# Kernel optimization log

Measured on AMD Instinct MI355X. Metric: run time of the kernel, lower is better.

The kernel has to match this reference:

```python
import jax, jax.numpy as jnp
import numpy as np

N_NODES = 10000
N_EDGES = 320000
IN_DIM = 128
HID = 256


def setup_inputs() -> dict:
    key = jax.random.key(0)
    ks = jax.random.split(key, 10)
    s_in = 1.0 / np.sqrt(IN_DIM)
    s_h = 1.0 / np.sqrt(HID)
    return {
        "x": jax.random.normal(ks[0], (N_NODES, IN_DIM), dtype=jnp.float32),
        "edge_index": jax.random.randint(ks[1], (2, N_EDGES), 0, N_NODES, dtype=jnp.int64),
        # feature_projector Linear(IN_DIM -> HID)
        "Wp": jax.random.uniform(ks[2], (IN_DIM, HID), jnp.float32, -s_in, s_in),
        "bp": jax.random.uniform(ks[3], (HID,), jnp.float32, -s_in, s_in),
        # LSTM(input=HID, hidden=HID) params, torch layout [4H, H], gate order i,f,g,o
        "W_ih": jax.random.uniform(ks[4], (4 * HID, HID), jnp.float32, -s_h, s_h),
        "W_hh": jax.random.uniform(ks[5], (4 * HID, HID), jnp.float32, -s_h, s_h),
        "b_ih": jax.random.uniform(ks[6], (4 * HID,), jnp.float32, -s_h, s_h),
        "b_hh": jax.random.uniform(ks[7], (4 * HID,), jnp.float32, -s_h, s_h),
        # EvolveGCN-O initial weight [H, H] (glorot-style)
        "initial_weight": jax.random.normal(ks[8], (HID, HID), dtype=jnp.float32) * np.sqrt(2.0 / (2 * HID)),
        # GCNConv bias
        "b_gcn": jnp.zeros((HID,), dtype=jnp.float32),
    }


def _forward(x, edge_index, Wp, bp, W_ih, W_hh, b_ih, b_hh, initial_weight, b_gcn):
    n = x.shape[0]
    # 1) feature projection
    h = x @ Wp + bp  # [N, H]
    # 2) EvolveGCN-O: one LSTM step on the weight matrix (rows = batch),
    #    with h0 = c0 = initial_weight; evolved hidden state is the GCN weight.
    gates = initial_weight @ W_ih.T + b_ih + initial_weight @ W_hh.T + b_hh  # [H, 4H]
    i_g, f_g, g_g, o_g = jnp.split(gates, 4, axis=-1)
    c = jax.nn.sigmoid(f_g) * initial_weight + jax.nn.sigmoid(i_g) * jnp.tanh(g_g)
    W = jax.nn.sigmoid(o_g) * jnp.tanh(c)  # [H, H]
    # 3) GCN propagation with fixed W: out = D^{-1/2}(A+I)D^{-1/2} (h W) + b
    hw = h @ W  # [N, H]
    self_loop = jnp.arange(n, dtype=edge_index.dtype)
    src = jnp.concatenate([edge_index[0], self_loop])
    dst = jnp.concatenate([edge_index[1], self_loop])
    ones = jnp.ones(src.shape[0], dtype=hw.dtype)
    deg = jax.ops.segment_sum(ones, dst, num_segments=n)  # in-degree incl. self loop
    dinv = jnp.where(deg > 0, jax.lax.rsqrt(deg), 0.0)
    norm = dinv[src] * dinv[dst]  # [E+N]
    out = jax.ops.segment_sum(hw[src] * norm[:, None], dst, num_segments=n)
    return out + b_gcn


def reference(x, edge_index, Wp, bp, W_ih, W_hh, b_ih, b_hh, initial_weight, b_gcn):
    return _forward(x, edge_index, Wp, bp, W_ih, W_hh, b_ih, b_hh, initial_weight, b_gcn)
```

## Files before the change

kernel.cpp:

```cpp
#include <hip/hip_runtime.h>
#include <math.h>

#define N_NODES 10000
#define N_EDGES 320000
#define IN_DIM  128
#define HID     256
#define CAP     128

#define NB_GATES 64
#define NB_FILL  1250
#define NB_XCVT  80


__device__ __forceinline__ unsigned bf16rne(float f) {
    union { float f; unsigned u; } c; c.f = f;
    return (c.u + 0x7FFFu + ((c.u >> 16) & 1u)) >> 16;
}

__global__ __launch_bounds__(256)
void k_prep(const int* __restrict__ ei, int* __restrict__ cursor,
            int* __restrict__ bucket, const float* __restrict__ iw,
            const float* __restrict__ wih, const float* __restrict__ whh,
            float* __restrict__ G, const float* __restrict__ x,
            unsigned* __restrict__ xb) {
    __shared__ float smem[8192];
    if (blockIdx.x >= NB_GATES + NB_FILL) {
        int tid = (blockIdx.x - NB_GATES - NB_FILL) * 256 + threadIdx.x;
        const float2* x2 = (const float2*)x;
        #pragma unroll
        for (int it = 0; it < 32; ++it) {
            int idx = tid + it * (NB_XCVT * 256);
            if (idx < N_NODES * 64) {
                float2 v = x2[idx];
                xb[idx] = bf16rne(v.x) | (bf16rne(v.y) << 16);
            }
        }
        return;
    }
    if (blockIdx.x >= NB_GATES) {
        int e = (blockIdx.x - NB_GATES) * 256 + threadIdx.x;
        int s = ei[e];
        int d = ei[N_EDGES + e];
        int pos = atomicAdd(&cursor[d], 1);
        if (pos < CAP) bucket[d * CAP + pos] = s;
        return;
    }
    int bid = blockIdx.x;
    int m0 = (bid & 3) * 64, n0 = (bid >> 2) * 64;
    float (*aT)[64] = (float(*)[64])smem;
    float (*bS)[64] = (float(*)[64])(smem + 4096);
    int t = threadIdx.x;
    int tm = t & 15, tn = t >> 4;
    float acc[4][4] = {};
    for (int kt = 0; kt < 4; ++kt) {
        int k0 = kt * 64;
        int row = t >> 2;
        #pragma unroll
        for (int r = 0; r < 4; ++r) {
            int k4 = 4 * (t & 3) + r;
            float4 av = *(const float4*)&iw[(m0 + row) * HID + k0 + 4 * k4];
            aT[4 * k4 + 0][row] = av.x; aT[4 * k4 + 1][row] = av.y;
            aT[4 * k4 + 2][row] = av.z; aT[4 * k4 + 3][row] = av.w;
            float4 b1 = *(const float4*)&wih[(n0 + row) * HID + k0 + 4 * k4];
            float4 b2 = *(const float4*)&whh[(n0 + row) * HID + k0 + 4 * k4];
            bS[4 * k4 + 0][row] = b1.x + b2.x; bS[4 * k4 + 1][row] = b1.y + b2.y;
            bS[4 * k4 + 2][row] = b1.z + b2.z; bS[4 * k4 + 3][row] = b1.w + b2.w;
        }
        __syncthreads();
        #pragma unroll 8
        for (int kk = 0; kk < 64; ++kk) {
            float4 a4 = *(const float4*)&aT[kk][4 * tm];
            float4 b4 = *(const float4*)&bS[kk][4 * tn];
            float a[4] = {a4.x, a4.y, a4.z, a4.w};
            float b[4] = {b4.x, b4.y, b4.z, b4.w};
            #pragma unroll
            for (int i = 0; i < 4; ++i)
                #pragma unroll
                for (int j = 0; j < 4; ++j)
                    acc[i][j] = fmaf(a[i], b[j], acc[i][j]);
        }
        __syncthreads();
    }
    #pragma unroll
    for (int i = 0; i < 4; ++i) {
        float4 o = make_float4(acc[i][0], acc[i][1], acc[i][2], acc[i][3]);
        *(float4*)&G[(m0 + 4 * tm + i) * 1024 + n0 + 4 * tn] = o;
    }
}

__global__ __launch_bounds__(256)
void k_wev(const float* __restrict__ G, const float* __restrict__ iw,
           const float* __restrict__ b_ih, const float* __restrict__ b_hh,
           float* __restrict__ Wev) {
    int r = blockIdx.x;
    int j = threadIdx.x;
    float gi = G[r * 1024 + 0   + j] + b_ih[0   + j] + b_hh[0   + j];
    float gf = G[r * 1024 + 256 + j] + b_ih[256 + j] + b_hh[256 + j];
    float gg = G[r * 1024 + 512 + j] + b_ih[512 + j] + b_hh[512 + j];
    float go = G[r * 1024 + 768 + j] + b_ih[768 + j] + b_hh[768 + j];
    float si = 1.f / (1.f + expf(-gi));
    float sf = 1.f / (1.f + expf(-gf));
    float so = 1.f / (1.f + expf(-go));
    float c  = sf * iw[r * HID + j] + si * tanhf(gg);
    Wev[r * HID + j] = so * tanhf(c);
}

__global__ __launch_bounds__(256)
void k_wc_agg(const unsigned* __restrict__ xb, const int* __restrict__ bucket,
              const int* __restrict__ cursor, float* __restrict__ y,
              float* __restrict__ rs, const float* __restrict__ Wp,
              const float* __restrict__ bp, const float* __restrict__ Wev,
              float* __restrict__ Wc, float* __restrict__ bc) {
    __shared__ float arow[HID];
    if (blockIdx.x < 129) {
        int a = blockIdx.x;
        int j = threadIdx.x;
        const float* srcRow = (a < IN_DIM) ? &Wp[a * HID] : bp;
        arow[j] = srcRow[j];
        __syncthreads();
        float acc = 0.f;
        #pragma unroll 4
        for (int k = 0; k < HID; ++k)
            acc = fmaf(arow[k], Wev[k * HID + j], acc);
        if (a < IN_DIM) Wc[a * HID + j] = acc;
        else            bc[j] = acc;
        return;
    }
    int wv   = threadIdx.x >> 6;
    int lane = threadIdx.x & 63;
    int v = (blockIdx.x - 129) * 4 + wv;
    int cntv = cursor[v];
    float dv = rsqrtf((float)(cntv + 1));
    int cnt = cntv > CAP ? CAP : cntv;
    unsigned self = xb[v * 64 + lane];
    union { unsigned u; float f; } c0, c1;
    c0.u = self << 16; c1.u = self & 0xFFFF0000u;
    float acc0 = dv * c0.f, acc1 = dv * c1.f;
    float wsum = dv;
    const int* bkt = &bucket[v * CAP];
    int j = 0;
    for (; j + 4 <= cnt; j += 4) {
        int s0 = bkt[j + 0], s1 = bkt[j + 1], s2 = bkt[j + 2], s3 = bkt[j + 3];
        float w0 = rsqrtf((float)(cursor[s0] + 1));
        float w1 = rsqrtf((float)(cursor[s1] + 1));
        float w2 = rsqrtf((float)(cursor[s2] + 1));
        float w3 = rsqrtf((float)(cursor[s3] + 1));
        unsigned r0 = xb[s0 * 64 + lane];
        unsigned r1 = xb[s1 * 64 + lane];
        unsigned r2 = xb[s2 * 64 + lane];
        unsigned r3 = xb[s3 * 64 + lane];
        union { unsigned u; float f; } a0, a1;
        a0.u = r0 << 16; a1.u = r0 & 0xFFFF0000u;
        acc0 = fmaf(w0, a0.f, acc0); acc1 = fmaf(w0, a1.f, acc1);
        a0.u = r1 << 16; a1.u = r1 & 0xFFFF0000u;
        acc0 = fmaf(w1, a0.f, acc0); acc1 = fmaf(w1, a1.f, acc1);
        a0.u = r2 << 16; a1.u = r2 & 0xFFFF0000u;
        acc0 = fmaf(w2, a0.f, acc0); acc1 = fmaf(w2, a1.f, acc1);
        a0.u = r3 << 16; a1.u = r3 & 0xFFFF0000u;
        acc0 = fmaf(w3, a0.f, acc0); acc1 = fmaf(w3, a1.f, acc1);
        wsum += w0 + w1 + w2 + w3;
    }
    for (; j < cnt; ++j) {
        int s = bkt[j];
        float w = rsqrtf((float)(cursor[s] + 1));
        unsigned r = xb[s * 64 + lane];
        union { unsigned u; float f; } a0, a1;
        a0.u = r << 16; a1.u = r & 0xFFFF0000u;
        acc0 = fmaf(w, a0.f, acc0); acc1 = fmaf(w, a1.f, acc1);
        wsum += w;
    }
    float2 o; o.x = dv * acc0; o.y = dv * acc1;
    ((float2*)y)[v * 64 + lane] = o;
    if (lane == 0) rs[v] = dv * wsum;
}

__global__ __launch_bounds__(256)
void k_out(const float* __restrict__ y, const float* __restrict__ Wc,
           const float* __restrict__ bc, const float* __restrict__ rs,
           const float* __restrict__ b_gcn, float* __restrict__ out) {
    __shared__ float yT[128][64];
    __shared__ float wcS[128][64];
    int m0 = blockIdx.x * 64, n0 = blockIdx.y * 64;
    int t = threadIdx.x;
    #pragma unroll
    for (int rr = 0; rr < 8; ++rr) {
        int p = t + 256 * rr;
        int k = p >> 4, n4 = p & 15;
        *(float4*)&wcS[k][4 * n4] = *(const float4*)&Wc[k * HID + n0 + 4 * n4];
    }
    int m = t >> 2;
    int gm = m0 + m;
    #pragma unroll
    for (int rr = 0; rr < 8; ++rr) {
        int k4 = 8 * (t & 3) + rr;
        float4 v = (gm < N_NODES) ? *(const float4*)&y[gm * IN_DIM + 4 * k4]
                                  : make_float4(0.f, 0.f, 0.f, 0.f);
        yT[4 * k4 + 0][m] = v.x; yT[4 * k4 + 1][m] = v.y;
        yT[4 * k4 + 2][m] = v.z; yT[4 * k4 + 3][m] = v.w;
    }
    __syncthreads();
    int tm = t & 15, tn = t >> 4;
    float acc[4][4] = {};
    #pragma unroll 4
    for (int k = 0; k < 128; ++k) {
        float4 a4 = *(const float4*)&yT[k][4 * tm];
        float4 b4 = *(const float4*)&wcS[k][4 * tn];
        float a[4] = {a4.x, a4.y, a4.z, a4.w};
        float b[4] = {b4.x, b4.y, b4.z, b4.w};
        #pragma unroll
        for (int i = 0; i < 4; ++i)
            #pragma unroll
            for (int j = 0; j < 4; ++j)
                acc[i][j] = fmaf(a[i], b[j], acc[i][j]);
    }
    float4 bcv = *(const float4*)&bc[n0 + 4 * tn];
    float4 bg  = *(const float4*)&b_gcn[n0 + 4 * tn];
    #pragma unroll
    for (int i = 0; i < 4; ++i) {
        int mm = m0 + 4 * tm + i;
        if (mm < N_NODES) {
            float rsv = rs[mm];
            float4 o;
            o.x = acc[i][0] + rsv * bcv.x + bg.x;
            o.y = acc[i][1] + rsv * bcv.y + bg.y;
            o.z = acc[i][2] + rsv * bcv.z + bg.z;
            o.w = acc[i][3] + rsv * bcv.w + bg.w;
            *(float4*)&out[mm * HID + n0 + 4 * tn] = o;
        }
    }
}

extern "C" void kernel_launch(void* const* d_in, const int* in_sizes, int n_in,
                              void* d_out, int out_size, void* d_ws, size_t ws_size,
                              hipStream_t stream) {
    const float* x     = (const float*)d_in[0];
    const int*   ei    = (const int*)d_in[1];
    const float* Wp    = (const float*)d_in[2];
    const float* bp    = (const float*)d_in[3];
    const float* W_ih  = (const float*)d_in[4];
    const float* W_hh  = (const float*)d_in[5];
    const float* b_ih  = (const float*)d_in[6];
    const float* b_hh  = (const float*)d_in[7];
    const float* iw    = (const float*)d_in[8];
    const float* b_gcn = (const float*)d_in[9];
    float* out = (float*)d_out;

    char* ws = (char*)d_ws;
    float*    y      = (float*)   (ws + 0);
    float*    G      = (float*)   (ws + 5120000);
    float*    Wev    = (float*)   (ws + 6168576);
    float*    Wc     = (float*)   (ws + 6430720);
    float*    bc     = (float*)   (ws + 6561792);
    float*    rs     = (float*)   (ws + 6562816);
    unsigned* xb     = (unsigned*)(ws + 6602816);
    int*      cursor = (int*)     (ws + 9162816);
    int*      bucket = (int*)     (ws + 9202816);

    hipMemsetAsync(cursor, 0, N_NODES * sizeof(int), stream);

    k_prep<<<NB_GATES + NB_FILL + NB_XCVT, 256, 0, stream>>>(
        ei, cursor, bucket, iw, W_ih, W_hh, G, x, xb);
    k_wev<<<256, 256, 0, stream>>>(G, iw, b_ih, b_hh, Wev);
    k_wc_agg<<<129 + 2500, 256, 0, stream>>>(xb, bucket, cursor, y, rs, Wp, bp, Wev, Wc, bc);
    k_out<<<dim3(157, 4), 256, 0, stream>>>(y, Wc, bc, rs, b_gcn, out);
}
```

Baseline: 152.8 us.

## Vectorize edge fill, precompute degree norms, widen output GEMM tile

The bucket-fill stage now reads four edges per thread with int4 loads, so it needs fewer blocks. Inverse-sqrt degrees are precomputed once into a dinv array inside the LSTM-gate kernel. The aggregation reads bucket indices as int4 and looks up dinv instead of recomputing rsqrt from cursor. The output GEMM switches to 64x128 tiles with 8x4 per-thread accumulators over two K chunks, which raises register use and halves the grid.

```diff
diff --git a/kernel.cpp b/kernel.cpp
--- a/kernel.cpp
+++ b/kernel.cpp
@@ -8,7 +8,7 @@
 #define CAP     128
 
 #define NB_GATES 64
-#define NB_FILL  1250
+#define NB_FILL  313
 #define NB_XCVT  80
 
 
@@ -38,11 +38,26 @@
         return;
     }
     if (blockIdx.x >= NB_GATES) {
-        int e = (blockIdx.x - NB_GATES) * 256 + threadIdx.x;
-        int s = ei[e];
-        int d = ei[N_EDGES + e];
-        int pos = atomicAdd(&cursor[d], 1);
-        if (pos < CAP) bucket[d * CAP + pos] = s;
+        int e = ((blockIdx.x - NB_GATES) * 256 + threadIdx.x) * 4;
+        if (e + 3 < N_EDGES) {
+            int4 s4 = *(const int4*)&ei[e];
+            int4 d4 = *(const int4*)&ei[N_EDGES + e];
+            int p0 = atomicAdd(&cursor[d4.x], 1);
+            if (p0 < CAP) bucket[d4.x * CAP + p0] = s4.x;
+            int p1 = atomicAdd(&cursor[d4.y], 1);
+            if (p1 < CAP) bucket[d4.y * CAP + p1] = s4.y;
+            int p2 = atomicAdd(&cursor[d4.z], 1);
+            if (p2 < CAP) bucket[d4.z * CAP + p2] = s4.z;
+            int p3 = atomicAdd(&cursor[d4.w], 1);
+            if (p3 < CAP) bucket[d4.w * CAP + p3] = s4.w;
+        } else {
+            for (int q = e; q < N_EDGES; ++q) {
+                int s = ei[q];
+                int d = ei[N_EDGES + q];
+                int pos = atomicAdd(&cursor[d], 1);
+                if (pos < CAP) bucket[d * CAP + pos] = s;
+            }
+        }
         return;
     }
     int bid = blockIdx.x;
@@ -89,9 +104,15 @@
 }
 
 __global__ __launch_bounds__(256)
-void k_wev(const float* __restrict__ G, const float* __restrict__ iw,
-           const float* __restrict__ b_ih, const float* __restrict__ b_hh,
-           float* __restrict__ Wev) {
+void k_wev_dinv(const float* __restrict__ G, const float* __restrict__ iw,
+                const float* __restrict__ b_ih, const float* __restrict__ b_hh,
+                float* __restrict__ Wev, const int* __restrict__ cursor,
+                float* __restrict__ dinv) {
+    if (blockIdx.x >= 256) {
+        int v = (blockIdx.x - 256) * 256 + threadIdx.x;
+        if (v < N_NODES) dinv[v] = rsqrtf((float)(cursor[v] + 1));
+        return;
+    }
     int r = blockIdx.x;
     int j = threadIdx.x;
     float gi = G[r * 1024 + 0   + j] + b_ih[0   + j] + b_hh[0   + j];
@@ -107,10 +128,11 @@
 
 __global__ __launch_bounds__(256)
 void k_wc_agg(const unsigned* __restrict__ xb, const int* __restrict__ bucket,
-              const int* __restrict__ cursor, float* __restrict__ y,
-              float* __restrict__ rs, const float* __restrict__ Wp,
-              const float* __restrict__ bp, const float* __restrict__ Wev,
-              float* __restrict__ Wc, float* __restrict__ bc) {
+              const int* __restrict__ cursor, const float* __restrict__ dinv,
+              float* __restrict__ y, float* __restrict__ rs,
+              const float* __restrict__ Wp, const float* __restrict__ bp,
+              const float* __restrict__ Wev, float* __restrict__ Wc,
+              float* __restrict__ bc) {
     __shared__ float arow[HID];
     if (blockIdx.x < 129) {
         int a = blockIdx.x;
@@ -130,25 +152,22 @@
     int lane = threadIdx.x & 63;
     int v = (blockIdx.x - 129) * 4 + wv;
     int cntv = cursor[v];
-    float dv = rsqrtf((float)(cntv + 1));
+    float dv = dinv[v];
     int cnt = cntv > CAP ? CAP : cntv;
     unsigned self = xb[v * 64 + lane];
     union { unsigned u; float f; } c0, c1;
     c0.u = self << 16; c1.u = self & 0xFFFF0000u;
     float acc0 = dv * c0.f, acc1 = dv * c1.f;
     float wsum = dv;
-    const int* bkt = &bucket[v * CAP];
+    const int4* bkt4 = (const int4*)&bucket[v * CAP];
     int j = 0;
     for (; j + 4 <= cnt; j += 4) {
-        int s0 = bkt[j + 0], s1 = bkt[j + 1], s2 = bkt[j + 2], s3 = bkt[j + 3];
-        float w0 = rsqrtf((float)(cursor[s0] + 1));
-        float w1 = rsqrtf((float)(cursor[s1] + 1));
-        float w2 = rsqrtf((float)(cursor[s2] + 1));
-        float w3 = rsqrtf((float)(cursor[s3] + 1));
-        unsigned r0 = xb[s0 * 64 + lane];
-        unsigned r1 = xb[s1 * 64 + lane];
-        unsigned r2 = xb[s2 * 64 + lane];
-        unsigned r3 = xb[s3 * 64 + lane];
+        int4 s = bkt4[j >> 2];
+        float w0 = dinv[s.x], w1 = dinv[s.y], w2 = dinv[s.z], w3 = dinv[s.w];
+        unsigned r0 = xb[s.x * 64 + lane];
+        unsigned r1 = xb[s.y * 64 + lane];
+        unsigned r2 = xb[s.z * 64 + lane];
+        unsigned r3 = xb[s.w * 64 + lane];
         union { unsigned u; float f; } a0, a1;
         a0.u = r0 << 16; a1.u = r0 & 0xFFFF0000u;
         acc0 = fmaf(w0, a0.f, acc0); acc1 = fmaf(w0, a1.f, acc1);
@@ -161,8 +180,8 @@
         wsum += w0 + w1 + w2 + w3;
     }
     for (; j < cnt; ++j) {
-        int s = bkt[j];
-        float w = rsqrtf((float)(cursor[s] + 1));
+        int s = ((const int*)bkt4)[j];
+        float w = dinv[s];
         unsigned r = xb[s * 64 + lane];
         union { unsigned u; float f; } a0, a1;
         a0.u = r << 16; a1.u = r & 0xFFFF0000u;
@@ -178,46 +197,56 @@
 void k_out(const float* __restrict__ y, const float* __restrict__ Wc,
            const float* __restrict__ bc, const float* __restrict__ rs,
            const float* __restrict__ b_gcn, float* __restrict__ out) {
-    __shared__ float yT[128][64];
-    __shared__ float wcS[128][64];
-    int m0 = blockIdx.x * 64, n0 = blockIdx.y * 64;
+    __shared__ float yT[64][64];
+    __shared__ float wcS[64][128];
+    int m0 = blockIdx.x * 64, n0 = blockIdx.y * 128;
     int t = threadIdx.x;
-    #pragma unroll
-    for (int rr = 0; rr < 8; ++rr) {
-        int p = t + 256 * rr;
-        int k = p >> 4, n4 = p & 15;
-        *(float4*)&wcS[k][4 * n4] = *(const float4*)&Wc[k * HID + n0 + 4 * n4];
-    }
-    int m = t >> 2;
-    int gm = m0 + m;
-    #pragma unroll
-    for (int rr = 0; rr < 8; ++rr) {
-        int k4 = 8 * (t & 3) + rr;
-        float4 v = (gm < N_NODES) ? *(const float4*)&y[gm * IN_DIM + 4 * k4]
-                                  : make_float4(0.f, 0.f, 0.f, 0.f);
-        yT[4 * k4 + 0][m] = v.x; yT[4 * k4 + 1][m] = v.y;
-        yT[4 * k4 + 2][m] = v.z; yT[4 * k4 + 3][m] = v.w;
-    }
-    __syncthreads();
-    int tm = t & 15, tn = t >> 4;
-    float acc[4][4] = {};
-    #pragma unroll 4
-    for (int k = 0; k < 128; ++k) {
-        float4 a4 = *(const float4*)&yT[k][4 * tm];
-        float4 b4 = *(const float4*)&wcS[k][4 * tn];
-        float a[4] = {a4.x, a4.y, a4.z, a4.w};
-        float b[4] = {b4.x, b4.y, b4.z, b4.w};
-        #pragma unroll
-        for (int i = 0; i < 4; ++i)
-            #pragma unroll
-            for (int j = 0; j < 4; ++j)
-                acc[i][j] = fmaf(a[i], b[j], acc[i][j]);
+    int tn = t & 31, tm = t >> 5;
+    float acc[8][4] = {};
+    for (int kc = 0; kc < 2; ++kc) {
+        {
+            int m = t >> 2, kq = t & 3;
+            int gm = m0 + m;
+            #pragma unroll
+            for (int r = 0; r < 4; ++r) {
+                int kk = kq * 16 + r * 4;
+                float4 v = (gm < N_NODES)
+                    ? *(const float4*)&y[gm * IN_DIM + kc * 64 + kk]
+                    : make_float4(0.f, 0.f, 0.f, 0.f);
+                yT[kk + 0][m] = v.x; yT[kk + 1][m] = v.y;
+                yT[kk + 2][m] = v.z; yT[kk + 3][m] = v.w;
+            }
+        }
+        {
+            int k = t >> 2, cq = t & 3;
+            #pragma unroll
+            for (int r = 0; r < 8; ++r) {
+                int col = 32 * cq + 4 * r;
+                *(float4*)&wcS[k][col] =
+                    *(const float4*)&Wc[(kc * 64 + k) * HID + n0 + col];
+            }
+        }
+        __syncthreads();
+        #pragma unroll 4
+        for (int k = 0; k < 64; ++k) {
+            float4 a0 = *(const float4*)&yT[k][8 * tm];
+            float4 a1 = *(const float4*)&yT[k][8 * tm + 4];
+            float4 b  = *(const float4*)&wcS[k][4 * tn];
+            float a[8] = {a0.x, a0.y, a0.z, a0.w, a1.x, a1.y, a1.z, a1.w};
+            float bb[4] = {b.x, b.y, b.z, b.w};
+            #pragma unroll
+            for (int i = 0; i < 8; ++i)
+                #pragma unroll
+                for (int j = 0; j < 4; ++j)
+                    acc[i][j] = fmaf(a[i], bb[j], acc[i][j]);
+        }
+        __syncthreads();
     }
     float4 bcv = *(const float4*)&bc[n0 + 4 * tn];
     float4 bg  = *(const float4*)&b_gcn[n0 + 4 * tn];
     #pragma unroll
-    for (int i = 0; i < 4; ++i) {
-        int mm = m0 + 4 * tm + i;
+    for (int i = 0; i < 8; ++i) {
+        int mm = m0 + 8 * tm + i;
         if (mm < N_NODES) {
             float rsv = rs[mm];
             float4 o;
@@ -254,13 +283,14 @@
     float*    rs     = (float*)   (ws + 6562816);
     unsigned* xb     = (unsigned*)(ws + 6602816);
     int*      cursor = (int*)     (ws + 9162816);
-    int*      bucket = (int*)     (ws + 9202816);
+    float*    dinv   = (float*)   (ws + 9202816);
+    int*      bucket = (int*)     (ws + 9242816);
 
     hipMemsetAsync(cursor, 0, N_NODES * sizeof(int), stream);
 
     k_prep<<<NB_GATES + NB_FILL + NB_XCVT, 256, 0, stream>>>(
         ei, cursor, bucket, iw, W_ih, W_hh, G, x, xb);
-    k_wev<<<256, 256, 0, stream>>>(G, iw, b_ih, b_hh, Wev);
-    k_wc_agg<<<129 + 2500, 256, 0, stream>>>(xb, bucket, cursor, y, rs, Wp, bp, Wev, Wc, bc);
-    k_out<<<dim3(157, 4), 256, 0, stream>>>(y, Wc, bc, rs, b_gcn, out);
-}
+    k_wev_dinv<<<256 + 40, 256, 0, stream>>>(G, iw, b_ih, b_hh, Wev, cursor, dinv);
+    k_wc_agg<<<129 + 2500, 256, 0, stream>>>(xb, bucket, cursor, dinv, y, rs, Wp, bp, Wev, Wc, bc);
+    k_out<<<dim3(157, 2), 256, 0, stream>>>(y, Wc, bc, rs, b_gcn, out);
+}
```

Measured after the change: 148.6 us. 1.03x faster.
